# Optimization experiments

Measured on AMD Instinct MI355X. Metric: run time of the kernel, lower is better.

Reference implementation:

```python
import jax, jax.numpy as jnp
import numpy as np

BN_EPS = 1e-5

def _bn_train(x, g, b):
    # BatchNorm1d in training mode: biased batch stats over the row dim
    m = x.mean(0)
    v = x.var(0)
    return g * (x - m) * jax.lax.rsqrt(v + BN_EPS) + b


def setup_inputs() -> dict:
    key = jax.random.key(0)
    ks = jax.random.split(key, 16)
    N, V, C, H, T, NC, OD, EH, EC = 128, 128, 256, 512, 12, 5, 5, 256, 256
    s = 0.05
    idx = jax.random.randint(ks[1], (T, N), 0, NC)
    return {
        "x": jax.random.normal(ks[0], (N, V, C), jnp.float32),
        "hidden_states": jnp.zeros((N, V, H), jnp.float32),
        "cell_states": jnp.zeros((N, V, H), jnp.float32),
        "one_hots_c_pred_seq": jax.nn.one_hot(idx, NC, dtype=jnp.float32),
        "W_ih": jax.random.normal(ks[2], (4 * H, C), jnp.float32) * s,
        "W_hh": jax.random.normal(ks[3], (4 * H, H), jnp.float32) * s,
        "b_ih": jax.random.normal(ks[4], (4 * H,), jnp.float32) * s,
        "b_hh": jax.random.normal(ks[5], (4 * H,), jnp.float32) * s,
        "W_cls": jax.random.normal(ks[6], (NC, H), jnp.float32) * s,
        "b_cls": jax.random.normal(ks[7], (NC,), jnp.float32) * s,
        "W_eh": jax.random.normal(ks[8], (EH, H), jnp.float32) * s,
        "b_eh": jax.random.normal(ks[9], (EH,), jnp.float32) * s,
        "g_eh": jnp.ones((EH,), jnp.float32),
        "beta_eh": jnp.zeros((EH,), jnp.float32),
        "W_ec": jax.random.normal(ks[10], (EC, NC), jnp.float32) * s,
        "b_ec": jax.random.normal(ks[11], (EC,), jnp.float32) * s,
        "g_ec": jnp.ones((EC,), jnp.float32),
        "beta_ec": jnp.zeros((EC,), jnp.float32),
        "W_out": jax.random.normal(ks[12], (OD, EH + EC), jnp.float32) * s,
        "b_out": jax.random.normal(ks[13], (OD,), jnp.float32) * s,
    }


def reference(x, hidden_states, cell_states, one_hots_c_pred_seq,
              W_ih, W_hh, b_ih, b_hh, W_cls, b_cls,
              W_eh, b_eh, g_eh, beta_eh, W_ec, b_ec, g_ec, beta_ec,
              W_out, b_out):
    N, V, C = x.shape
    H = hidden_states.shape[-1]
    xf = x.reshape(N * V, C)
    gx = xf @ W_ih.T + b_ih  # input gates are identical every step (x is repeated)

    def step(carry, onehot):
        h, c = carry  # [N*V, H]
        gates = gx + h @ W_hh.T + b_hh
        i, f, g, o = jnp.split(gates, 4, axis=1)  # pytorch LSTMCell gate order
        c = jax.nn.sigmoid(f) * c + jax.nn.sigmoid(i) * jnp.tanh(g)
        h = jax.nn.sigmoid(o) * jnp.tanh(c)
        # ClassifierLayer: avg-pool over V then 1x1 conv == mean + linear
        oc = h.reshape(N, V, H).mean(1) @ W_cls.T + b_cls  # [N, nc]
        # PredictionLayer
        eh = jax.nn.relu(_bn_train(h @ W_eh.T + b_eh, g_eh, beta_eh))
        ohr = jnp.broadcast_to(onehot[:, None, :], (N, V, onehot.shape[-1])).reshape(N * V, -1)
        ec = jax.nn.relu(_bn_train(ohr @ W_ec.T + b_ec, g_ec, beta_ec))
        op = jnp.concatenate([eh, ec], axis=1) @ W_out.T + b_out  # [N*V, out_dim]
        return (h, c), (op.reshape(N, V, -1), oc)

    carry0 = (hidden_states.reshape(N * V, H), cell_states.reshape(N * V, H))
    _, (preds, c_outs) = jax.lax.scan(step, carry0, one_hots_c_pred_seq)
    preds = preds.transpose(1, 0, 2, 3)  # [N, T, V, out_dim]
    # output_activation: bivariate-Gaussian params
    pred_outs = jnp.stack([preds[..., 0], preds[..., 1],
                           jnp.exp(preds[..., 2]), jnp.exp(preds[..., 3]),
                           jnp.tanh(preds[..., 4])], axis=-1)
    return pred_outs, c_outs
```

## Files before the change

kernel.cpp:

```cpp
#include <hip/hip_runtime.h>
#include <hip/hip_bf16.h>
#include <stdint.h>

typedef __hip_bfloat16 bf16;
typedef __attribute__((ext_vector_type(8))) short bf16x8;
typedef __attribute__((ext_vector_type(4))) short bf16x4;
typedef __attribute__((ext_vector_type(4))) float f32x4;

#define NN 128
#define VV 128
#define CC 256
#define HH 512
#define TT 12
#define NCLS 5
#define OD 5
#define EHD 256
#define KCAT (HH + CC)
#define ROWS (NN * VV)
#define PRED_SZ (NN * TT * VV * OD)
#define LDP 72
#define MiB (1ull << 20)


__device__ __forceinline__ float sigm(float x) {
    return __builtin_amdgcn_rcpf(1.f + __expf(-x));
}
__device__ __forceinline__ float tanh_(float x) {
    x = fminf(fmaxf(x, -15.f), 15.f);
    float e = __expf(2.f * x);
    return (e - 1.f) * __builtin_amdgcn_rcpf(e + 1.f);
}
__device__ __forceinline__ float bf2f(unsigned short v) {
    unsigned u = ((unsigned)v) << 16; float f; __builtin_memcpy(&f, &u, 4); return f;
}
__device__ __forceinline__ float ldin(const void* p, int i, int is32) {
    return is32 ? ((const float*)p)[i] : __bfloat162float(((const bf16*)p)[i]);
}

__device__ __forceinline__ void gl_lds16(const bf16* g, bf16* l) {
    __builtin_amdgcn_global_load_lds(
        (const __attribute__((address_space(1))) unsigned int*)g,
        (__attribute__((address_space(3))) unsigned int*)l, 16, 0, 0);
}
__device__ __forceinline__ void stage128(const bf16* __restrict__ A, int lda, int row0,
                                         const bf16* __restrict__ B, int ldb, int col0,
                                         int k, bf16* As, bf16* Bs) {
    int lane = threadIdx.x & 63, wave = threadIdx.x >> 6;
    const bf16* pA = A + (size_t)(row0 + wave * 32 + (lane >> 3)) * lda + k + (lane & 7) * 8;
    const bf16* pB = B + (size_t)(col0 + wave * 32 + (lane >> 3)) * ldb + k + (lane & 7) * 8;
    bf16* lA = As + wave * 2048 + lane * 8;
    bf16* lB = Bs + wave * 2048 + lane * 8;
#pragma unroll
    for (int j = 0; j < 4; ++j) {
        gl_lds16(pA + (size_t)(j * 8) * lda, lA + j * 512);
        gl_lds16(pB + (size_t)(j * 8) * ldb, lB + j * 512);
    }
}
__device__ __forceinline__ void tile_mfma64(const bf16* As, const bf16* Bs, f32x4 acc[4][4]) {
    const int lane = threadIdx.x & 63, wave = threadIdx.x >> 6;
    const int wro = (wave >> 1) * 64, wco = (wave & 1) * 64;
    const int l15 = lane & 15, l8 = (lane >> 4) * 8;
#pragma unroll
    for (int kk = 0; kk < 64; kk += 32) {
        bf16x8 af[4], bg[4];
#pragma unroll
        for (int x = 0; x < 4; ++x) {
            af[x] = *(const bf16x8*)(As + (wro + x * 16 + l15) * 64 + kk + l8);
            bg[x] = *(const bf16x8*)(Bs + (wco + x * 16 + l15) * 64 + kk + l8);
        }
#pragma unroll
        for (int bi = 0; bi < 4; ++bi)
#pragma unroll
            for (int bj = 0; bj < 4; ++bj)
                acc[bi][bj] = __builtin_amdgcn_mfma_f32_16x16x32_bf16(af[bi], bg[bj], acc[bi][bj], 0, 0, 0);
    }
}

__global__ void detect_dtype(const void* g_eh, int* flag, int* hnz) {
    unsigned w = *(const unsigned*)g_eh;
    *flag = (w == 0x3F800000u) ? 1 : 0;
    *hnz = 0;
}

__global__ __launch_bounds__(256) void convert_in(const void* src, bf16* dst, int n, const int* flag) {
    int is32 = *flag;
    int i = blockIdx.x * 256 + threadIdx.x;
    int stride = gridDim.x * 256;
    if (is32) { const float* s = (const float*)src; for (; i < n; i += stride) dst[i] = __float2bfloat16(s[i]); }
    else      { const bf16*  s = (const bf16*)src;  for (; i < n; i += stride) dst[i] = s[i]; }
}

__global__ __launch_bounds__(256) void convert_in_hflag(const void* src, bf16* dst, int n, const int* flag,
                                                        int* nz) {
    int is32 = *flag;
    int i = blockIdx.x * 256 + threadIdx.x;
    int stride = gridDim.x * 256;
    int loc = 0;
    if (is32) {
        const float* s = (const float*)src;
        for (; i < n; i += stride) { float v = s[i]; if (__float_as_uint(v) != 0u) loc = 1; dst[i] = __float2bfloat16(v); }
    } else {
        const bf16* s = (const bf16*)src;
        for (; i < n; i += stride) { bf16 v = s[i]; if (*(const unsigned short*)&v) loc = 1; dst[i] = v; }
    }
    if (loc) atomicOr(nz, 1);
}

__global__ __launch_bounds__(256) void init_c(const void* cell, bf16* c, const int* flag) {
    int is32 = *flag;
    size_t i = (size_t)blockIdx.x * 256 + threadIdx.x;
    const size_t total = (size_t)ROWS * HH;
    for (; i < total; i += (size_t)8192 * 256) c[i] = __float2bfloat16(ldin(cell, (int)i, is32));
}

__device__ __forceinline__ void issue_loads(const bf16* __restrict__ A, int lda, int row0, int ka,
                                            const bf16* __restrict__ B, int ldb, int col0, int kb,
                                            bf16x8 ar[4], bf16x8 br[4]) {
    int tid = threadIdx.x;
#pragma unroll
    for (int it = 0; it < 4; ++it) {
        int cidx = tid + 256 * it;
        int row = cidx >> 3;
        int cc8 = (cidx & 7) * 8;
        ar[it] = *(const bf16x8*)(A + (size_t)(row0 + row) * lda + ka + cc8);
        br[it] = *(const bf16x8*)(B + (size_t)(col0 + row) * ldb + kb + cc8);
    }
}
__device__ __forceinline__ void write_lds(bf16* As, bf16* Bs, const bf16x8 ar[4], const bf16x8 br[4]) {
    int tid = threadIdx.x;
#pragma unroll
    for (int it = 0; it < 4; ++it) {
        int cidx = tid + 256 * it;
        int row = cidx >> 3;
        int cc8 = (cidx & 7) * 8;
        *(bf16x8*)(As + row * LDP + cc8) = ar[it];
        *(bf16x8*)(Bs + row * LDP + cc8) = br[it];
    }
}
__device__ __forceinline__ void tile_mfma(const bf16* As, const bf16* Bs, f32x4 acc[4][4]) {
    const int lane = threadIdx.x & 63, wave = threadIdx.x >> 6;
    const int wro = (wave >> 1) * 64, wco = (wave & 1) * 64;
    const int l15 = lane & 15, l8 = (lane >> 4) * 8;
#pragma unroll
    for (int kk = 0; kk < 64; kk += 32) {
        bf16x8 af[4], bg[4];
#pragma unroll
        for (int x = 0; x < 4; ++x) {
            af[x] = *(const bf16x8*)(As + (wro + x * 16 + l15) * LDP + kk + l8);
            bg[x] = *(const bf16x8*)(Bs + (wco + x * 16 + l15) * LDP + kk + l8);
        }
#pragma unroll
        for (int bi = 0; bi < 4; ++bi)
#pragma unroll
            for (int bj = 0; bj < 4; ++bj)
                acc[bi][bj] = __builtin_amdgcn_mfma_f32_16x16x32_bf16(af[bi], bg[bj], acc[bi][bj], 0, 0, 0);
    }
}

__global__ __launch_bounds__(256) void prep_weights(const void* __restrict__ Wih, const void* __restrict__ Whh,
                                                    const void* __restrict__ bih, const void* __restrict__ bhh,
                                                    bf16* __restrict__ Wihp, bf16* __restrict__ Whhp,
                                                    float* __restrict__ biasp, const int* flag) {
    int is32 = *flag;
    int jg = blockIdx.x;
    int b = jg >> 7, j = jg & 127;
    int gate = (j >> 4) & 3;
    int unit = b * 32 + (j & 15) + 16 * (j >> 6);
    int p = gate * HH + unit;
    for (int k = threadIdx.x; k < HH; k += 256)
        Whhp[(size_t)jg * HH + k] = __float2bfloat16(ldin(Whh, p * HH + k, is32));
    for (int k = threadIdx.x; k < CC; k += 256)
        Wihp[(size_t)jg * CC + k] = __float2bfloat16(ldin(Wih, p * CC + k, is32));
    if (threadIdx.x == 0)
        biasp[jg] = ldin(bih, p, is32) + ldin(bhh, p, is32);
}

__global__ __launch_bounds__(256) void gemm_k0(const bf16* __restrict__ A, const bf16* __restrict__ B,
                                               const float* __restrict__ biasp, bf16* __restrict__ gx) {
    __shared__ bf16 As[128 * 64], Bs[128 * 64];
    f32x4 acc[4][4] = {};
    int row0 = blockIdx.x * 128, col0 = blockIdx.y * 128;
    for (int k0 = 0; k0 < CC; k0 += 64) {
        __syncthreads();
        stage128(A, CC, row0, B, CC, col0, k0, As, Bs);
        __syncthreads();
        tile_mfma64(As, Bs, acc);
    }
    int lane = threadIdx.x & 63, wave = threadIdx.x >> 6;
    int wro = (wave >> 1) * 64, wco = (wave & 1) * 64;
    int l15 = lane & 15, lr4 = (lane >> 4) * 4;
#pragma unroll
    for (int bj = 0; bj < 4; ++bj) {
        int j = wco + bj * 16 + l15;
        float bia = biasp[col0 + j];
        int sidx = wco + l15 * 4 + bj;
#pragma unroll
        for (int bi = 0; bi < 4; ++bi)
#pragma unroll
            for (int reg = 0; reg < 4; ++reg) {
                int r = row0 + wro + bi * 16 + lr4 + reg;
                gx[(size_t)r * 2048 + col0 + sidx] = __float2bfloat16(acc[bi][bj][reg] + bia);
            }
    }
}

__global__ __launch_bounds__(256) void ec_precompute(const void* __restrict__ W_ec, const void* __restrict__ b_ec,
                                                     const void* __restrict__ g_ec, const void* __restrict__ beta_ec,
                                                     const void* __restrict__ W_out, const void* __restrict__ b_out,
                                                     const void* __restrict__ onehot, float* __restrict__ ecd_all,
                                                     const int* flag) {
    __shared__ float ecv[NCLS][EHD];
    __shared__ float cntf[NCLS];
    __shared__ float ecdc[NCLS][OD];
    int is32 = *flag;
    int t = blockIdx.x, tid = threadIdx.x;
    int ohoff = t * NN * NCLS;
    if (tid < NCLS) {
        float cnum = 0.f;
        for (int n = 0; n < NN; ++n) cnum += ldin(onehot, ohoff + n * NCLS + tid, is32);
        cntf[tid] = cnum * (1.f / NN);
    }
    __syncthreads();
    {
        int j = tid;
        float vals[NCLS];
        float m = 0.f, e2 = 0.f;
        float be = ldin(b_ec, j, is32);
        for (int cc = 0; cc < NCLS; ++cc) {
            vals[cc] = ldin(W_ec, j * NCLS + cc, is32) + be;
            m += cntf[cc] * vals[cc];
            e2 += cntf[cc] * vals[cc] * vals[cc];
        }
        float rs = rsqrtf(e2 - m * m + 1e-5f);
        float g = ldin(g_ec, j, is32), bt = ldin(beta_ec, j, is32);
        for (int cc = 0; cc < NCLS; ++cc)
            ecv[cc][j] = fmaxf(g * (vals[cc] - m) * rs + bt, 0.f);
    }
    __syncthreads();
    if (tid < NCLS * OD) {
        int cc = tid / OD, k = tid % OD;
        float s = 0.f;
        for (int j = 0; j < EHD; ++j) s += ecv[cc][j] * ldin(W_out, k * (EHD * 2) + EHD + j, is32);
        ecdc[cc][k] = s;
    }
    __syncthreads();
    if (tid < NN) {
        for (int k = 0; k < OD; ++k) {
            float s = ldin(b_out, k, is32);
            for (int cc = 0; cc < NCLS; ++cc) s += ldin(onehot, ohoff + tid * NCLS + cc, is32) * ecdc[cc][k];
            ecd_all[((size_t)t * NN + tid) * OD + k] = s;
        }
    }
}

__device__ __forceinline__ void final_rows(int grp, const bf16* __restrict__ ehp, const float* __restrict__ colsum,
                                           const float* __restrict__ colss, const void* __restrict__ g_eh,
                                           const void* __restrict__ beta_eh, const float* __restrict__ ecd_all,
                                           const float* Wl, void* __restrict__ out, int t, int is32) {
    int wave = threadIdx.x >> 6, lane = threadIdx.x & 63;
    int r = grp * 4 + wave;
    int j0 = lane * 4;
    float av[4], bv[4];
#pragma unroll
    for (int e = 0; e < 4; ++e) {
        float mean = colsum[j0 + e] * (1.f / ROWS);
        float var = colss[j0 + e] * (1.f / ROWS) - mean * mean;
        float a = ldin(g_eh, j0 + e, is32) * rsqrtf(var + 1e-5f);
        av[e] = a;
        bv[e] = ldin(beta_eh, j0 + e, is32) - mean * a;
    }
    bf16x4 xs = *(const bf16x4*)(ehp + (size_t)r * EHD + j0);
    float v0 = fmaxf(av[0] * bf2f((unsigned short)xs[0]) + bv[0], 0.f);
    float v1 = fmaxf(av[1] * bf2f((unsigned short)xs[1]) + bv[1], 0.f);
    float v2 = fmaxf(av[2] * bf2f((unsigned short)xs[2]) + bv[2], 0.f);
    float v3 = fmaxf(av[3] * bf2f((unsigned short)xs[3]) + bv[3], 0.f);
    float p[OD];
#pragma unroll
    for (int k = 0; k < OD; ++k)
        p[k] = v0 * Wl[k * EHD + j0] + v1 * Wl[k * EHD + j0 + 1] + v2 * Wl[k * EHD + j0 + 2] + v3 * Wl[k * EHD + j0 + 3];
#pragma unroll
    for (int off = 32; off; off >>= 1)
#pragma unroll
        for (int k = 0; k < OD; ++k) p[k] += __shfl_down(p[k], off, 64);
    if (lane == 0) {
        int n = r >> 7, v = r & 127;
        const float* en = ecd_all + ((size_t)t * NN + n) * OD;
        float o0 = p[0] + en[0];
        float o1 = p[1] + en[1];
        float o2 = expf(p[2] + en[2]);
        float o3 = expf(p[3] + en[3]);
        float o4 = tanh_(p[4] + en[4]);
        size_t base = (size_t)n * (TT * VV * OD) + (size_t)t * (VV * OD) + (size_t)v * OD;
        if (is32) {
            float* dst = (float*)out + base;
            dst[0] = o0; dst[1] = o1; dst[2] = o2; dst[3] = o3; dst[4] = o4;
        } else {
            bf16* dst = (bf16*)out + base;
            dst[0] = __float2bfloat16(o0);
            dst[1] = __float2bfloat16(o1);
            dst[2] = __float2bfloat16(o2);
            dst[3] = __float2bfloat16(o3);
            dst[4] = __float2bfloat16(o4);
        }
    }
}

__global__ __launch_bounds__(256) void lstm_fused(const bf16* __restrict__ h_in, const bf16* __restrict__ Whhp,
                                                  const bf16* __restrict__ gx, bf16* __restrict__ c,
                                                  bf16* __restrict__ h_out, float* __restrict__ csum_cur,
                                                  float* __restrict__ colsum_z, float* __restrict__ colss_z,
                                                  const bf16* __restrict__ Weh, const void* __restrict__ b_eh,
                                                  bf16* __restrict__ ehp_w, float* __restrict__ colsum_w,
                                                  float* __restrict__ colss_w, const float* __restrict__ csum_prev,
                                                  const void* __restrict__ W_cls, const void* __restrict__ b_cls,
                                                  void* __restrict__ outp, int t_aux,
                                                  const bf16* __restrict__ ehp_r, const float* __restrict__ colsum_r,
                                                  const float* __restrict__ colss_r, const void* __restrict__ g_eh,
                                                  const void* __restrict__ beta_eh, const void* __restrict__ W_out,
                                                  const float* __restrict__ ecd_all, int t_final,
                                                  const int* __restrict__ flag) {
    __shared__ __align__(16) unsigned char smem[32768];
    int tid = threadIdx.x;
    if (blockIdx.x < 2048) {
        bf16* As = (bf16*)smem;
        bf16* Bs = (bf16*)(smem + 16384);
        f32x4 acc[4][4] = {};
        bf16x4 gpre[16];
        unsigned short cpre[16];
        int row0 = (blockIdx.x & 127) * 128, col0 = (blockIdx.x >> 7) * 128;
        int lane = tid & 63, wave = tid >> 6;
        int wro = (wave >> 1) * 64;
        int l15 = lane & 15, lr4 = (lane >> 4) * 4;
        int ul = (wave & 1) * 16 + l15;
        int u = (blockIdx.x >> 7) * 32 + ul;
        const bf16* gxp = gx + col0 + (wave & 1) * 64 + l15 * 4;
#pragma unroll
        for (int k0 = 0; k0 < HH; k0 += 64) {
            __syncthreads();
            stage128(h_in, HH, row0, Whhp, HH, col0, k0, As, Bs);
            __syncthreads();
#pragma unroll
            for (int e = 0; e < 2; ++e) {
                int idx = (k0 >> 6) * 2 + e;
                int bi = idx >> 2, reg = idx & 3;
                int r = row0 + wro + bi * 16 + lr4 + reg;
                gpre[idx] = *(const bf16x4*)(gxp + (size_t)r * 2048);
                cpre[idx] = *(const unsigned short*)(c + (size_t)r * HH + u);
            }
            tile_mfma64(As, Bs, acc);
        }
        __syncthreads();
        float* hsum = (float*)smem;
        if (tid < 32) hsum[tid] = 0.f;
        if (blockIdx.x == 0) { colsum_z[tid] = 0.f; colss_z[tid] = 0.f; }
        __syncthreads();
        float hpart = 0.f;
#pragma unroll
        for (int bi = 0; bi < 4; ++bi) {
#pragma unroll
            for (int reg = 0; reg < 4; ++reg) {
                int idx = bi * 4 + reg;
                int r = row0 + wro + bi * 16 + lr4 + reg;
                float gi = acc[bi][0][reg] + bf2f((unsigned short)gpre[idx][0]);
                float gf = acc[bi][1][reg] + bf2f((unsigned short)gpre[idx][1]);
                float gg = acc[bi][2][reg] + bf2f((unsigned short)gpre[idx][2]);
                float go = acc[bi][3][reg] + bf2f((unsigned short)gpre[idx][3]);
                float iv = sigm(gi), fv = sigm(gf), gv = tanh_(gg), ov = sigm(go);
                size_t ci = (size_t)r * HH + u;
                float cn = fv * bf2f(cpre[idx]) + iv * gv;
                c[ci] = __float2bfloat16(cn);
                float hv = ov * tanh_(cn);
                h_out[ci] = __float2bfloat16(hv);
                hpart += hv;
            }
        }
        atomicAdd(&hsum[ul], hpart);
        __syncthreads();
        if (tid < 32) csum_cur[(size_t)(blockIdx.x & 127) * HH + (blockIdx.x >> 7) * 32 + tid] = hsum[tid];
        return;
    }
    int is32 = *flag;
    int b = blockIdx.x - 2048;
    if (b >= 640) {
        if (t_final < 0) return;
        float* Wl = (float*)smem;
        for (int i = tid; i < OD * EHD; i += 256)
            Wl[i] = ldin(W_out, (i >> 8) * (EHD * 2) + (i & 255), is32);
        __syncthreads();
        int fb = b - 640;
#pragma unroll
        for (int g = 0; g < 4; ++g)
            final_rows(fb * 4 + g, ehp_r, colsum_r, colss_r, g_eh, beta_eh, ecd_all, Wl, outp, t_final, is32);
        return;
    }
    if (b >= 512) {
        if (t_aux < 0) return;
        float* wl = (float*)smem;
        float* wred = (float*)(smem + 10240);
        int wave = tid >> 6, lane = tid & 63;
        for (int i = tid; i < NCLS * HH; i += 256) wl[i] = ldin(W_cls, i, is32);
        __syncthreads();
        int n = b - 512;
        float pk[NCLS] = {};
        for (int u = tid; u < HH; u += 256) {
            float cv = csum_prev[(size_t)n * HH + u];
#pragma unroll
            for (int k = 0; k < NCLS; ++k) pk[k] += cv * wl[k * HH + u];
        }
#pragma unroll
        for (int off = 32; off; off >>= 1)
#pragma unroll
            for (int k = 0; k < NCLS; ++k) pk[k] += __shfl_down(pk[k], off, 64);
        if (lane == 0)
#pragma unroll
            for (int k = 0; k < NCLS; ++k) wred[wave * NCLS + k] = pk[k];
        __syncthreads();
        if (tid < NCLS) {
            float a = (wred[tid] + wred[NCLS + tid] + wred[2 * NCLS + tid] + wred[3 * NCLS + tid]) * (1.f / VV)
                      + ldin(b_cls, tid, is32);
            int idx = PRED_SZ + t_aux * (NN * NCLS) + n * NCLS + tid;
            if (is32) ((float*)outp)[idx] = a;
            else      ((bf16*)outp)[idx] = __float2bfloat16(a);
        }
        return;
    }
    if (t_aux < 0) return;
    bf16* As = (bf16*)smem;
    bf16* Bs = (bf16*)(smem + 8192);
    float* s_sum = (float*)(smem + 24576);
    float* s_ss  = (float*)(smem + 25088);
    f32x4 acc[4][2] = {};
    int row0 = (b >> 1) * 64, col0 = (b & 1) * 128;
    const int lane = tid & 63, wave = tid >> 6;
    const int l15 = lane & 15, l8 = (lane >> 4) * 8;
    const bf16* pA = h_in + (size_t)(row0 + wave * 16 + (lane >> 3)) * HH + (lane & 7) * 8;
    const bf16* pB = Weh + (size_t)(col0 + wave * 32 + (lane >> 3)) * HH + (lane & 7) * 8;
    bf16* lA = As + wave * 1024 + lane * 8;
    bf16* lB = Bs + wave * 2048 + lane * 8;
    for (int k0 = 0; k0 < HH; k0 += 64) {
        __syncthreads();
        gl_lds16(pA + k0, lA);
        gl_lds16(pA + 8 * HH + k0, lA + 512);
#pragma unroll
        for (int j = 0; j < 4; ++j) gl_lds16(pB + (size_t)(j * 8) * HH + k0, lB + j * 512);
        __syncthreads();
#pragma unroll
        for (int kk = 0; kk < 64; kk += 32) {
            bf16x8 af[4], bg[2];
#pragma unroll
            for (int x = 0; x < 4; ++x) af[x] = *(const bf16x8*)(As + (x * 16 + l15) * 64 + kk + l8);
#pragma unroll
            for (int x = 0; x < 2; ++x) bg[x] = *(const bf16x8*)(Bs + (wave * 32 + x * 16 + l15) * 64 + kk + l8);
#pragma unroll
            for (int bi = 0; bi < 4; ++bi)
#pragma unroll
                for (int bj = 0; bj < 2; ++bj)
                    acc[bi][bj] = __builtin_amdgcn_mfma_f32_16x16x32_bf16(af[bi], bg[bj], acc[bi][bj], 0, 0, 0);
        }
    }
    int lr4 = (lane >> 4) * 4;
    if (tid < 128) { s_sum[tid] = 0.f; s_ss[tid] = 0.f; }
    __syncthreads();
#pragma unroll
    for (int bj = 0; bj < 2; ++bj) {
        int j = wave * 32 + bj * 16 + l15;
        int col = col0 + j;
        float bia = ldin(b_eh, col, is32);
        float ps = 0.f, pss = 0.f;
#pragma unroll
        for (int bi = 0; bi < 4; ++bi)
#pragma unroll
            for (int reg = 0; reg < 4; ++reg) {
                int r = row0 + bi * 16 + lr4 + reg;
                float val = acc[bi][bj][reg] + bia;
                ehp_w[(size_t)r * EHD + col] = __float2bfloat16(val);
                ps += val; pss += val * val;
            }
        atomicAdd(&s_sum[j], ps);
        atomicAdd(&s_ss[j], pss);
    }
    __syncthreads();
    if (tid < 128) {
        atomicAdd(&colsum_w[col0 + tid], s_sum[tid]);
        atomicAdd(&colss_w[col0 + tid], s_ss[tid]);
    }
}

__global__ __launch_bounds__(256) void lstm_gemm_gx_first(const bf16* __restrict__ h_in, const bf16* __restrict__ Whhp,
                                                          const bf16* __restrict__ gx, bf16* __restrict__ c,
                                                          bf16* __restrict__ h_out, float* __restrict__ csum,
                                                          float* __restrict__ colsum, float* __restrict__ colss,
                                                          const int* __restrict__ gemm_flag) {
    __shared__ bf16 As[128 * 64], Bs[128 * 64];
    __shared__ float hsum[32];
    f32x4 acc[4][4] = {};
    bf16x4 gpre[16];
    unsigned short cpre[16];
    int row0 = blockIdx.x * 128, col0 = blockIdx.y * 128;
    int tid = threadIdx.x, lane = tid & 63, wave = tid >> 6;
    int wro = (wave >> 1) * 64;
    int l15 = lane & 15, lr4 = (lane >> 4) * 4;
    int ul = (wave & 1) * 16 + l15;
    int u = blockIdx.y * 32 + ul;
    const bf16* gxp = gx + col0 + (wave & 1) * 64 + l15 * 4;
    const int do_gemm = *gemm_flag;
    if (do_gemm) {
#pragma unroll
        for (int k0 = 0; k0 < HH; k0 += 64) {
            __syncthreads();
            stage128(h_in, HH, row0, Whhp, HH, col0, k0, As, Bs);
            __syncthreads();
#pragma unroll
            for (int e = 0; e < 2; ++e) {
                int idx = (k0 >> 6) * 2 + e;
                int bi = idx >> 2, reg = idx & 3;
                int r = row0 + wro + bi * 16 + lr4 + reg;
                gpre[idx] = *(const bf16x4*)(gxp + (size_t)r * 2048);
                cpre[idx] = *(const unsigned short*)(c + (size_t)r * HH + u);
            }
            tile_mfma64(As, Bs, acc);
        }
    } else {
#pragma unroll
        for (int idx = 0; idx < 16; ++idx) {
            int bi = idx >> 2, reg = idx & 3;
            int r = row0 + wro + bi * 16 + lr4 + reg;
            gpre[idx] = *(const bf16x4*)(gxp + (size_t)r * 2048);
            cpre[idx] = *(const unsigned short*)(c + (size_t)r * HH + u);
        }
    }
    __syncthreads();
    if (tid < 32) hsum[tid] = 0.f;
    if (blockIdx.x == 0 && blockIdx.y == 0) { colsum[tid] = 0.f; colss[tid] = 0.f; }
    __syncthreads();
    float hpart = 0.f;
#pragma unroll
    for (int bi = 0; bi < 4; ++bi) {
#pragma unroll
        for (int reg = 0; reg < 4; ++reg) {
            int idx = bi * 4 + reg;
            int r = row0 + wro + bi * 16 + lr4 + reg;
            float gi = acc[bi][0][reg] + bf2f((unsigned short)gpre[idx][0]);
            float gf = acc[bi][1][reg] + bf2f((unsigned short)gpre[idx][1]);
            float gg = acc[bi][2][reg] + bf2f((unsigned short)gpre[idx][2]);
            float go = acc[bi][3][reg] + bf2f((unsigned short)gpre[idx][3]);
            float iv = sigm(gi), fv = sigm(gf), gv = tanh_(gg), ov = sigm(go);
            size_t ci = (size_t)r * HH + u;
            float cn = fv * bf2f(cpre[idx]) + iv * gv;
            c[ci] = __float2bfloat16(cn);
            float hv = ov * tanh_(cn);
            h_out[ci] = __float2bfloat16(hv);
            hpart += hv;
        }
    }
    atomicAdd(&hsum[ul], hpart);
    __syncthreads();
    if (tid < 32) csum[(size_t)blockIdx.x * HH + blockIdx.y * 32 + tid] = hsum[tid];
}

__global__ __launch_bounds__(256) void lstm_gemm_cat(const bf16* __restrict__ h_in, const bf16* __restrict__ x,
                                                     const bf16* __restrict__ Wihp, const bf16* __restrict__ Whhp,
                                                     const float* __restrict__ biasp, bf16* __restrict__ c,
                                                     bf16* __restrict__ h_out, float* __restrict__ csum,
                                                     float* __restrict__ colsum, float* __restrict__ colss) {
    __shared__ bf16 As[128 * LDP], Bs[128 * LDP];
    __shared__ float hsum[32];
    f32x4 acc[4][4] = {};
    bf16x8 ar[4], br[4];
    int row0 = blockIdx.x * 128, col0 = blockIdx.y * 128;
    issue_loads(h_in, HH, row0, 0, Whhp, HH, col0, 0, ar, br);
    for (int k0 = 0; k0 < KCAT; k0 += 64) {
        __syncthreads();
        write_lds(As, Bs, ar, br);
        __syncthreads();
        int kn = k0 + 64;
        if (kn < KCAT) {
            if (kn < HH) issue_loads(h_in, HH, row0, kn, Whhp, HH, col0, kn, ar, br);
            else         issue_loads(x, CC, row0, kn - HH, Wihp, CC, col0, kn - HH, ar, br);
        }
        tile_mfma(As, Bs, acc);
    }
    int tid = threadIdx.x;
    if (tid < 32) hsum[tid] = 0.f;
    if (blockIdx.x == 0 && blockIdx.y == 0) { colsum[tid] = 0.f; colss[tid] = 0.f; }
    __syncthreads();
    int lane = tid & 63, wave = tid >> 6;
    int wro = (wave >> 1) * 64;
    int l15 = lane & 15, lr4 = (lane >> 4) * 4;
    int ul = (wave & 1) * 16 + l15;
    int u = blockIdx.y * 32 + ul;
    int colp = col0 + (wave & 1) * 64 + l15;
    float b0 = biasp[colp], b1 = biasp[colp + 16], b2 = biasp[colp + 32], b3 = biasp[colp + 48];
    float hpart = 0.f;
#pragma unroll
    for (int bi = 0; bi < 4; ++bi) {
#pragma unroll
        for (int reg = 0; reg < 4; ++reg) {
            int r = row0 + wro + bi * 16 + lr4 + reg;
            float gi = acc[bi][0][reg] + b0;
            float gf = acc[bi][1][reg] + b1;
            float gg = acc[bi][2][reg] + b2;
            float go = acc[bi][3][reg] + b3;
            float iv = sigm(gi), fv = sigm(gf), gv = tanh_(gg), ov = sigm(go);
            size_t ci = (size_t)r * HH + u;
            float cn = fv * __bfloat162float(c[ci]) + iv * gv;
            c[ci] = __float2bfloat16(cn);
            float hv = ov * tanh_(cn);
            h_out[ci] = __float2bfloat16(hv);
            hpart += hv;
        }
    }
    atomicAdd(&hsum[ul], hpart);
    __syncthreads();
    if (tid < 32) csum[(size_t)blockIdx.x * HH + blockIdx.y * 32 + tid] = hsum[tid];
}

__global__ __launch_bounds__(256) void eh_cls(const bf16* __restrict__ A, const bf16* __restrict__ B,
                                              const void* __restrict__ bias, bf16* __restrict__ out,
                                              float* __restrict__ colsum, float* __restrict__ colss,
                                              const float* __restrict__ csum, const void* __restrict__ W_cls,
                                              const void* __restrict__ b_cls, void* __restrict__ outp,
                                              int t, const int* flag,
                                              const bf16* __restrict__ ehp_prev, const float* __restrict__ colsum_prev,
                                              const float* __restrict__ colss_prev, const void* __restrict__ g_eh,
                                              const void* __restrict__ beta_eh, const void* __restrict__ W_out,
                                              const float* __restrict__ ecd_all, int tprev) {
    __shared__ __align__(16) unsigned char smem[32768];
    int is32 = *flag;
    int tid = threadIdx.x;
    if (blockIdx.x >= 640) {
        if (tprev < 0) return;
        float* Wl = (float*)smem;
        for (int i = tid; i < OD * EHD; i += 256)
            Wl[i] = ldin(W_out, (i >> 8) * (EHD * 2) + (i & 255), is32);
        __syncthreads();
        int fb = blockIdx.x - 640;
#pragma unroll
        for (int g = 0; g < 4; ++g)
            final_rows(fb * 4 + g, ehp_prev, colsum_prev, colss_prev, g_eh, beta_eh,
                       ecd_all, Wl, outp, tprev, is32);
        return;
    }
    if (blockIdx.x >= 512) {
        float* wl = (float*)smem;
        float* wred = (float*)(smem + 10240);
        int wave = tid >> 6, lane = tid & 63;
        for (int i = tid; i < NCLS * HH; i += 256) wl[i] = ldin(W_cls, i, is32);
        __syncthreads();
        int n = blockIdx.x - 512;
        float pk[NCLS] = {};
        for (int u = tid; u < HH; u += 256) {
            float cv = csum[(size_t)n * HH + u];
#pragma unroll
            for (int k = 0; k < NCLS; ++k) pk[k] += cv * wl[k * HH + u];
        }
#pragma unroll
        for (int off = 32; off; off >>= 1)
#pragma unroll
            for (int k = 0; k < NCLS; ++k) pk[k] += __shfl_down(pk[k], off, 64);
        if (lane == 0)
#pragma unroll
            for (int k = 0; k < NCLS; ++k) wred[wave * NCLS + k] = pk[k];
        __syncthreads();
        if (tid < NCLS) {
            float a = (wred[tid] + wred[NCLS + tid] + wred[2 * NCLS + tid] + wred[3 * NCLS + tid]) * (1.f / VV)
                      + ldin(b_cls, tid, is32);
            int idx = PRED_SZ + t * (NN * NCLS) + n * NCLS + tid;
            if (is32) ((float*)outp)[idx] = a;
            else      ((bf16*)outp)[idx] = __float2bfloat16(a);
        }
        return;
    }
    bf16* As = (bf16*)smem;
    bf16* Bs = (bf16*)(smem + 8192);
    float* s_sum = (float*)(smem + 24576);
    float* s_ss  = (float*)(smem + 25088);
    f32x4 acc[4][2] = {};
    int row0 = (blockIdx.x >> 1) * 64, col0 = (blockIdx.x & 1) * 128;
    const int lane = tid & 63, wave = tid >> 6;
    const int l15 = lane & 15, l8 = (lane >> 4) * 8;
    const bf16* pA = A + (size_t)(row0 + wave * 16 + (lane >> 3)) * HH + (lane & 7) * 8;
    const bf16* pB = B + (size_t)(col0 + wave * 32 + (lane >> 3)) * HH + (lane & 7) * 8;
    bf16* lA = As + wave * 1024 + lane * 8;
    bf16* lB = Bs + wave * 2048 + lane * 8;
    for (int k0 = 0; k0 < HH; k0 += 64) {
        __syncthreads();
        gl_lds16(pA + k0, lA);
        gl_lds16(pA + 8 * HH + k0, lA + 512);
#pragma unroll
        for (int j = 0; j < 4; ++j) gl_lds16(pB + (size_t)(j * 8) * HH + k0, lB + j * 512);
        __syncthreads();
#pragma unroll
        for (int kk = 0; kk < 64; kk += 32) {
            bf16x8 af[4], bg[2];
#pragma unroll
            for (int x = 0; x < 4; ++x) af[x] = *(const bf16x8*)(As + (x * 16 + l15) * 64 + kk + l8);
#pragma unroll
            for (int x = 0; x < 2; ++x) bg[x] = *(const bf16x8*)(Bs + (wave * 32 + x * 16 + l15) * 64 + kk + l8);
#pragma unroll
            for (int bi = 0; bi < 4; ++bi)
#pragma unroll
                for (int bj = 0; bj < 2; ++bj)
                    acc[bi][bj] = __builtin_amdgcn_mfma_f32_16x16x32_bf16(af[bi], bg[bj], acc[bi][bj], 0, 0, 0);
        }
    }
    int lr4 = (lane >> 4) * 4;
    if (tid < 128) { s_sum[tid] = 0.f; s_ss[tid] = 0.f; }
    __syncthreads();
#pragma unroll
    for (int bj = 0; bj < 2; ++bj) {
        int j = wave * 32 + bj * 16 + l15;
        int col = col0 + j;
        float bia = ldin(bias, col, is32);
        float ps = 0.f, pss = 0.f;
#pragma unroll
        for (int bi = 0; bi < 4; ++bi)
#pragma unroll
            for (int reg = 0; reg < 4; ++reg) {
                int r = row0 + bi * 16 + lr4 + reg;
                float val = acc[bi][bj][reg] + bia;
                out[(size_t)r * EHD + col] = __float2bfloat16(val);
                ps += val; pss += val * val;
            }
        atomicAdd(&s_sum[j], ps);
        atomicAdd(&s_ss[j], pss);
    }
    __syncthreads();
    if (tid < 128) {
        atomicAdd(&colsum[col0 + tid], s_sum[tid]);
        atomicAdd(&colss[col0 + tid], s_ss[tid]);
    }
}

__global__ __launch_bounds__(256) void final_kernel(const bf16* __restrict__ eh_pre, const float* __restrict__ colsum,
                                                    const float* __restrict__ colss, const void* __restrict__ g_eh,
                                                    const void* __restrict__ beta_eh, const void* __restrict__ W_out,
                                                    const float* __restrict__ ecd_all, void* __restrict__ out,
                                                    int t, const int* flag) {
    __shared__ float Wl[OD * EHD];
    int is32 = *flag;
    for (int i = threadIdx.x; i < OD * EHD; i += 256)
        Wl[i] = ldin(W_out, (i >> 8) * (EHD * 2) + (i & 255), is32);
    __syncthreads();
    final_rows(blockIdx.x, eh_pre, colsum, colss, g_eh, beta_eh, ecd_all, Wl, out, t, is32);
}

extern "C" void kernel_launch(void* const* d_in, const int* in_sizes, int n_in,
                              void* d_out, int out_size, void* d_ws, size_t ws_size,
                              hipStream_t stream) {
    const void* x       = d_in[0];
    const void* hidden  = d_in[1];
    const void* cell    = d_in[2];
    const void* onehot  = d_in[3];
    const void* W_ih    = d_in[4];
    const void* W_hh    = d_in[5];
    const void* b_ih    = d_in[6];
    const void* b_hh    = d_in[7];
    const void* W_cls   = d_in[8];
    const void* b_cls   = d_in[9];
    const void* W_eh    = d_in[10];
    const void* b_eh    = d_in[11];
    const void* g_eh    = d_in[12];
    const void* beta_eh = d_in[13];
    const void* W_ec    = d_in[14];
    const void* b_ec    = d_in[15];
    const void* g_ec    = d_in[16];
    const void* beta_ec = d_in[17];
    const void* W_out   = d_in[18];
    const void* b_out   = d_in[19];

    const int use_gx = (ws_size >= 148 * MiB) ? 1 : 0;

    char* ws = (char*)d_ws;
    bf16*  cbuf = (bf16*)(ws);
    char*  tail = ws + 16 * MiB;
    bf16*  h0   = (bf16*)(ws + 32 * MiB);
    bf16*  h1   = (bf16*)(ws + 48 * MiB);
    bf16*  gxb  = (bf16*)(ws + 64 * MiB);
    bf16*  ehp0, *ehp1, *x_c, *Wihp, *Whhp, *Weh_c;
    if (use_gx) {
        ehp0  = (bf16*)(ws + 128 * MiB);
        x_c   = (bf16*)(ws + 136 * MiB);
        ehp1  = (bf16*)(ws + 136 * MiB);
        Wihp  = (bf16*)(ws + 144 * MiB);
        Whhp  = (bf16*)(ws + 145 * MiB);
        Weh_c = (bf16*)(ws + 147 * MiB);
    } else {
        ehp0  = (bf16*)(ws + 64 * MiB);
        x_c   = (bf16*)(ws + 72 * MiB);
        ehp1  = (bf16*)(ws + 80 * MiB);
        Wihp  = (bf16*)(ws + 88 * MiB);
        Whhp  = (bf16*)(ws + 89 * MiB);
        Weh_c = (bf16*)(ws + 91 * MiB);
    }
    float* biasp   = (float*)(tail);
    float* colsum3[3] = { (float*)(tail + 8192), (float*)(tail + 10240), (float*)(tail + 12288) };
    float* colss3[3]  = { (float*)(tail + 9216), (float*)(tail + 11264), (float*)(tail + 13312) };
    int*   dflag   = (int*)  (tail + 16384);
    int*   hnz     = (int*)  (tail + 16388);
    float* csum0   = (float*)(tail + 20480);
    float* csum1   = (float*)(tail + 20480 + 262144);
    float* ecd_all = (float*)(tail + 20480 + 524288);

    bf16*  ehp_b[2]  = { ehp0, ehp1 };
    float* csum_b[2] = { csum0, csum1 };

    detect_dtype<<<1, 1, 0, stream>>>(g_eh, dflag, hnz);
    convert_in<<<4096, 256, 0, stream>>>(x, x_c, ROWS * CC, dflag);
    convert_in_hflag<<<4096, 256, 0, stream>>>(hidden, h0, ROWS * HH, dflag, hnz);
    convert_in<<<512, 256, 0, stream>>>(W_eh, Weh_c, EHD * HH, dflag);
    init_c<<<8192, 256, 0, stream>>>(cell, cbuf, dflag);
    prep_weights<<<2048, 256, 0, stream>>>(W_ih, W_hh, b_ih, b_hh, Wihp, Whhp, biasp, dflag);
    ec_precompute<<<TT, 256, 0, stream>>>(W_ec, b_ec, g_ec, beta_ec, W_out, b_out, onehot, ecd_all, dflag);
    if (use_gx)
        gemm_k0<<<dim3(128, 16), 256, 0, stream>>>(x_c, Wihp, biasp, gxb);

    if (use_gx) {
        lstm_gemm_gx_first<<<dim3(128, 16), 256, 0, stream>>>(h0, Whhp, gxb, cbuf, h1, csum_b[0],
                                                              colsum3[0], colss3[0], hnz);
        for (int t = 1; t < TT; ++t) {
            const bf16* hin = (t & 1) ? h1 : h0;
            bf16* hout = (t & 1) ? h0 : h1;
            int tp = t - 1, tf = t - 2;
            lstm_fused<<<3712, 256, 0, stream>>>(
                hin, Whhp, gxb, cbuf, hout, csum_b[t & 1], colsum3[t % 3], colss3[t % 3],
                Weh_c, b_eh, ehp_b[tp & 1], colsum3[tp % 3], colss3[tp % 3], csum_b[tp & 1],
                W_cls, b_cls, d_out, tp,
                ehp_b[t & 1] , colsum3[(tf + 3) % 3], colss3[(tf + 3) % 3],
                g_eh, beta_eh, W_out, ecd_all, tf, dflag);
        }
        {
            int t = TT - 1;
            const bf16* h_last = (t & 1) ? h1 : h0;
            eh_cls<<<1664, 256, 0, stream>>>(h_last, Weh_c, b_eh, ehp_b[t & 1], colsum3[t % 3], colss3[t % 3],
                                             csum_b[t & 1], W_cls, b_cls, d_out, t, dflag,
                                             ehp_b[(t - 1) & 1], colsum3[(t - 1) % 3], colss3[(t - 1) % 3],
                                             g_eh, beta_eh, W_out, ecd_all, t - 1);
            final_kernel<<<4096, 256, 0, stream>>>(ehp_b[t & 1], colsum3[t % 3], colss3[t % 3],
                                                   g_eh, beta_eh, W_out, ecd_all, d_out, t, dflag);
        }
    } else {
        for (int t = 0; t < TT; ++t) {
            const bf16* hin = (t & 1) ? h1 : h0;
            bf16* hout = (t & 1) ? h0 : h1;
            lstm_gemm_cat<<<dim3(128, 16), 256, 0, stream>>>(hin, x_c, Wihp, Whhp, biasp, cbuf, hout,
                                                             csum_b[t & 1], colsum3[t % 3], colss3[t % 3]);
            eh_cls<<<1664, 256, 0, stream>>>(hout, Weh_c, b_eh, ehp_b[t & 1], colsum3[t % 3], colss3[t % 3],
                                             csum_b[t & 1], W_cls, b_cls, d_out, t, dflag,
                                             ehp_b[(t - 1) & 1], colsum3[((t - 1) + 3) % 3], colss3[((t - 1) + 3) % 3],
                                             g_eh, beta_eh, W_out, ecd_all, t - 1);
        }
        final_kernel<<<4096, 256, 0, stream>>>(ehp_b[(TT - 1) & 1], colsum3[(TT - 1) % 3], colss3[(TT - 1) % 3],
                                               g_eh, beta_eh, W_out, ecd_all, d_out, TT - 1, dflag);
    }
}
```

Before: 1.222 ms.

## Double-buffer LDS staging with XOR-swizzled layout in recurrent and eh GEMMs

Replaces the single-buffered K=64 staging loops in the LSTM recurrent GEMM and the eh projection GEMM with double-buffered K=32 stages. The next tile is prefetched into the alternate LDS buffer while MFMAs run on the current one, and one barrier per stage replaces two. It also adds an XOR swizzle to the LDS layout to reduce bank conflicts on fragment reads. The cost is more iterations with smaller stages and more complex address arithmetic. The eh path's buffer reassignment must also stay clear of the s_sum/s_ss region.

```diff
diff --git a/kernel.cpp b/kernel.cpp
--- a/kernel.cpp
+++ b/kernel.cpp
@@ -42,6 +42,52 @@
         (const __attribute__((address_space(1))) unsigned int*)g,
         (__attribute__((address_space(3))) unsigned int*)l, 16, 0, 0);
 }
+
+
+__device__ __forceinline__ void stage_t128s(const bf16* __restrict__ g, int ldg, int row0, int k0,
+                                            bf16* lds) {
+    int lane = threadIdx.x & 63, wave = threadIdx.x >> 6;
+#pragma unroll
+    for (int j = 0; j < 2; ++j) {
+        int slot = j * 256 + wave * 64 + lane;
+        int lds_row = slot >> 3;
+        int bx = ((slot & 7) * 16) ^ ((lds_row & 7) << 4);
+        int r = lds_row + 64 * (bx >> 6);
+        int cb = bx & 63;
+        gl_lds16(g + (size_t)(row0 + r) * ldg + k0 + (cb >> 1), lds + slot * 8);
+    }
+}
+__device__ __forceinline__ void stage_t64s(const bf16* __restrict__ g, int ldg, int row0, int k0,
+                                           bf16* lds) {
+    int lane = threadIdx.x & 63, wave = threadIdx.x >> 6;
+    int slot = wave * 64 + lane;
+    int lds_row = slot >> 3;
+    int bx = ((slot & 7) * 16) ^ ((lds_row & 7) << 4);
+    int r = lds_row + 32 * (bx >> 6);
+    int cb = bx & 63;
+    gl_lds16(g + (size_t)(row0 + r) * ldg + k0 + (cb >> 1), lds + slot * 8);
+}
+__device__ __forceinline__ bf16x8 swz_rd(const bf16* base, int lds_row, int half, int eb) {
+    int off = lds_row * 128 + ((half * 64 + eb) ^ ((lds_row & 7) << 4));
+    return *(const bf16x8*)((const char*)base + off);
+}
+__device__ __forceinline__ void mfma_step32(const bf16* As, const bf16* Bs, f32x4 acc[4][4]) {
+    const int lane = threadIdx.x & 63, wave = threadIdx.x >> 6;
+    const int ha = wave >> 1, hb = wave & 1;
+    const int l15 = lane & 15, eb = (lane >> 4) * 16;
+    bf16x8 af[4], bg[4];
+#pragma unroll
+    for (int x = 0; x < 4; ++x) {
+        af[x] = swz_rd(As, x * 16 + l15, ha, eb);
+        bg[x] = swz_rd(Bs, x * 16 + l15, hb, eb);
+    }
+#pragma unroll
+    for (int bi = 0; bi < 4; ++bi)
+#pragma unroll
+        for (int bj = 0; bj < 4; ++bj)
+            acc[bi][bj] = __builtin_amdgcn_mfma_f32_16x16x32_bf16(af[bi], bg[bj], acc[bi][bj], 0, 0, 0);
+}
+
 __device__ __forceinline__ void stage128(const bf16* __restrict__ A, int lda, int row0,
                                          const bf16* __restrict__ B, int ldb, int col0,
                                          int k, bf16* As, bf16* Bs) {
@@ -322,8 +368,10 @@
     __shared__ __align__(16) unsigned char smem[32768];
     int tid = threadIdx.x;
     if (blockIdx.x < 2048) {
-        bf16* As = (bf16*)smem;
-        bf16* Bs = (bf16*)(smem + 16384);
+        bf16* As0 = (bf16*)smem;
+        bf16* As1 = (bf16*)(smem + 8192);
+        bf16* Bs0 = (bf16*)(smem + 16384);
+        bf16* Bs1 = (bf16*)(smem + 24576);
         f32x4 acc[4][4] = {};
         bf16x4 gpre[16];
         unsigned short cpre[16];
@@ -334,22 +382,28 @@
         int ul = (wave & 1) * 16 + l15;
         int u = (blockIdx.x >> 7) * 32 + ul;
         const bf16* gxp = gx + col0 + (wave & 1) * 64 + l15 * 4;
-#pragma unroll
-        for (int k0 = 0; k0 < HH; k0 += 64) {
+        stage_t128s(h_in, HH, row0, 0, As0);
+        stage_t128s(Whhp, HH, col0, 0, Bs0);
+        __syncthreads();
+#pragma unroll
+        for (int s = 0; s < 16; ++s) {
+            const bf16* Ac = (s & 1) ? As1 : As0;
+            const bf16* Bc = (s & 1) ? Bs1 : Bs0;
+            bf16* An = (s & 1) ? As0 : As1;
+            bf16* Bn = (s & 1) ? Bs0 : Bs1;
+            if (s < 15) {
+                stage_t128s(h_in, HH, row0, (s + 1) * 32, An);
+                stage_t128s(Whhp, HH, col0, (s + 1) * 32, Bn);
+            }
+            {
+                int bi = s >> 2, reg = s & 3;
+                int r = row0 + wro + bi * 16 + lr4 + reg;
+                gpre[s] = *(const bf16x4*)(gxp + (size_t)r * 2048);
+                cpre[s] = *(const unsigned short*)(c + (size_t)r * HH + u);
+            }
+            mfma_step32(Ac, Bc, acc);
             __syncthreads();
-            stage128(h_in, HH, row0, Whhp, HH, col0, k0, As, Bs);
-            __syncthreads();
-#pragma unroll
-            for (int e = 0; e < 2; ++e) {
-                int idx = (k0 >> 6) * 2 + e;
-                int bi = idx >> 2, reg = idx & 3;
-                int r = row0 + wro + bi * 16 + lr4 + reg;
-                gpre[idx] = *(const bf16x4*)(gxp + (size_t)r * 2048);
-                cpre[idx] = *(const unsigned short*)(c + (size_t)r * HH + u);
-            }
-            tile_mfma64(As, Bs, acc);
-        }
-        __syncthreads();
+        }
         float* hsum = (float*)smem;
         if (tid < 32) hsum[tid] = 0.f;
         if (blockIdx.x == 0) { colsum_z[tid] = 0.f; colss_z[tid] = 0.f; }
@@ -425,38 +479,42 @@
         return;
     }
     if (t_aux < 0) return;
-    bf16* As = (bf16*)smem;
-    bf16* Bs = (bf16*)(smem + 8192);
+    bf16* As0 = (bf16*)smem;
+    bf16* As1 = (bf16*)(smem + 4096);
+    bf16* Bs0 = (bf16*)(smem + 8192);
+    bf16* Bs1 = (bf16*)(smem + 16384);
     float* s_sum = (float*)(smem + 24576);
     float* s_ss  = (float*)(smem + 25088);
     f32x4 acc[4][2] = {};
     int row0 = (b >> 1) * 64, col0 = (b & 1) * 128;
     const int lane = tid & 63, wave = tid >> 6;
-    const int l15 = lane & 15, l8 = (lane >> 4) * 8;
-    const bf16* pA = h_in + (size_t)(row0 + wave * 16 + (lane >> 3)) * HH + (lane & 7) * 8;
-    const bf16* pB = Weh + (size_t)(col0 + wave * 32 + (lane >> 3)) * HH + (lane & 7) * 8;
-    bf16* lA = As + wave * 1024 + lane * 8;
-    bf16* lB = Bs + wave * 2048 + lane * 8;
-    for (int k0 = 0; k0 < HH; k0 += 64) {
-        __syncthreads();
-        gl_lds16(pA + k0, lA);
-        gl_lds16(pA + 8 * HH + k0, lA + 512);
-#pragma unroll
-        for (int j = 0; j < 4; ++j) gl_lds16(pB + (size_t)(j * 8) * HH + k0, lB + j * 512);
-        __syncthreads();
-#pragma unroll
-        for (int kk = 0; kk < 64; kk += 32) {
-            bf16x8 af[4], bg[2];
-#pragma unroll
-            for (int x = 0; x < 4; ++x) af[x] = *(const bf16x8*)(As + (x * 16 + l15) * 64 + kk + l8);
-#pragma unroll
-            for (int x = 0; x < 2; ++x) bg[x] = *(const bf16x8*)(Bs + (wave * 32 + x * 16 + l15) * 64 + kk + l8);
-#pragma unroll
-            for (int bi = 0; bi < 4; ++bi)
-#pragma unroll
-                for (int bj = 0; bj < 2; ++bj)
-                    acc[bi][bj] = __builtin_amdgcn_mfma_f32_16x16x32_bf16(af[bi], bg[bj], acc[bi][bj], 0, 0, 0);
-        }
+    const int l15 = lane & 15, eb = (lane >> 4) * 16;
+    stage_t64s(h_in, HH, row0, 0, As0);
+    stage_t128s(Weh, HH, col0, 0, Bs0);
+    __syncthreads();
+#pragma unroll
+    for (int s = 0; s < 16; ++s) {
+        const bf16* Ac = (s & 1) ? As1 : As0;
+        const bf16* Bc = (s & 1) ? Bs1 : Bs0;
+        bf16* An = (s & 1) ? As0 : As1;
+        bf16* Bn = (s & 1) ? Bs0 : Bs1;
+        if (s < 15) {
+            stage_t64s(h_in, HH, row0, (s + 1) * 32, An);
+            stage_t128s(Weh, HH, col0, (s + 1) * 32, Bn);
+        }
+        bf16x8 af[4], bg[2];
+#pragma unroll
+        for (int x = 0; x < 4; ++x)
+            af[x] = swz_rd(Ac, (x & 1) * 16 + l15, x >> 1, eb);
+#pragma unroll
+        for (int x = 0; x < 2; ++x)
+            bg[x] = swz_rd(Bc, (wave & 1) * 32 + x * 16 + l15, wave >> 1, eb);
+#pragma unroll
+        for (int bi = 0; bi < 4; ++bi)
+#pragma unroll
+            for (int bj = 0; bj < 2; ++bj)
+                acc[bi][bj] = __builtin_amdgcn_mfma_f32_16x16x32_bf16(af[bi], bg[bj], acc[bi][bj], 0, 0, 0);
+        __syncthreads();
     }
     int lr4 = (lane >> 4) * 4;
     if (tid < 128) { s_sum[tid] = 0.f; s_ss[tid] = 0.f; }
```

Result: no change. 1.243 ms (+1.7%).
